# Kernel optimization log

Hardware: AMD Instinct MI355X
Metric: run time of the kernel (lower is better)

The kernel has to match this reference:

```python
import jax, jax.numpy as jnp
import numpy as np

B, N = 16, 2048
NOTE, BEAT_H, MEAS_H, FINAL_H = 512, 128, 64, 128
NUM_BEATS, NUM_MEAS = 256, 64
OUT = 11            # output_size; QPM_INDEX = 0
QPM = 0


def _uniform(k, shape, fan):
    b = 1.0 / np.sqrt(fan)
    return jax.random.uniform(k, shape, jnp.float32, -b, b)


def _lstm_cell(x, h, c, wih, whh, bih, bhh):
    g = x @ wih.T + bih + h @ whh.T + bhh
    ii, ff, gg, oo = jnp.split(g, 4, axis=-1)
    c2 = jax.nn.sigmoid(ff) * c + jax.nn.sigmoid(ii) * jnp.tanh(gg)
    return jax.nn.sigmoid(oo) * jnp.tanh(c2), c2


def setup_inputs() -> dict:
    key = jax.random.key(0)
    ks = jax.random.split(key, 20)
    note_emb = jax.random.normal(ks[0], (B, N, NOTE), jnp.float32)
    beat_emb = jax.random.normal(ks[1], (B, NUM_BEATS, BEAT_H), jnp.float32)
    measure_emb = jax.random.normal(ks[2], (B, NUM_MEAS, MEAS_H), jnp.float32)
    beat_numbers = jnp.sort(jax.random.randint(ks[3], (B, N), 0, NUM_BEATS), axis=1)
    measure_numbers = beat_numbers // (NUM_BEATS // NUM_MEAS)
    tin = BEAT_H + MEAS_H + 1 + (OUT - 1)   # beat-tempo LSTM input size
    fin = NOTE + BEAT_H + MEAS_H + OUT      # final LSTM input size
    d = OUT - 1
    return {
        "note_emb": note_emb, "beat_emb": beat_emb, "measure_emb": measure_emb,
        "beat_numbers": beat_numbers, "measure_numbers": measure_numbers,
        "Wa": _uniform(ks[4], (d, d), d), "ba": _uniform(ks[5], (d,), d),
        "ctx": _uniform(ks[6], (d,), d),
        "Wih_t": _uniform(ks[7], (4 * BEAT_H, tin), BEAT_H),
        "Whh_t": _uniform(ks[8], (4 * BEAT_H, BEAT_H), BEAT_H),
        "bih_t": _uniform(ks[9], (4 * BEAT_H,), BEAT_H),
        "bhh_t": _uniform(ks[10], (4 * BEAT_H,), BEAT_H),
        "Wih_f": _uniform(ks[11], (4 * FINAL_H, fin), FINAL_H),
        "Whh_f": _uniform(ks[12], (4 * FINAL_H, FINAL_H), FINAL_H),
        "bih_f": _uniform(ks[13], (4 * FINAL_H,), FINAL_H),
        "bhh_f": _uniform(ks[14], (4 * FINAL_H,), FINAL_H),
        "W_fc": _uniform(ks[15], (d, FINAL_H), FINAL_H),
        "b_fc": _uniform(ks[16], (d,), FINAL_H),
        "W_tfc": _uniform(ks[17], (1, BEAT_H), BEAT_H),
        "b_tfc": _uniform(ks[18], (1,), BEAT_H),
    }


def _decode(note_emb, beat_emb, measure_emb, beat_numbers, measure_numbers,
            Wa, ba, ctx, Wih_t, Whh_t, bih_t, bhh_t,
            Wih_f, Whh_f, bih_f, bhh_f, W_fc, b_fc, W_tfc, b_tfc):
    Bn, Nn = note_emb.shape[0], note_emb.shape[1]
    d = W_fc.shape[0]  # OUT - 1
    zs_beat = jnp.maximum(beat_numbers - beat_numbers[:, :1], 0)
    zs_meas = jnp.maximum(measure_numbers - measure_numbers[:, :1], 0)
    diff = jnp.diff(beat_numbers, axis=1)
    # beat_changed: first step forced to 1, then diff of beat numbers
    changed_all = jnp.concatenate([jnp.ones((Bn, 1), diff.dtype), diff], axis=1) > 0
    pos = jnp.arange(Nn)
    bidx = jnp.arange(Bn)

    carry0 = (
        jnp.zeros((Bn, BEAT_H)), jnp.zeros((Bn, BEAT_H)),        # tempo h, c
        jnp.zeros((Bn, FINAL_H)), jnp.zeros((Bn, FINAL_H)),      # final h, c
        jnp.zeros((Bn, d + 1)),                                   # prev_out
        jnp.zeros((Bn, beat_emb.shape[1], d)),                    # beat_results
        jnp.zeros((Bn, Nn, d + 1)),                               # out_total
    )

    def step(carry, i):
        th, tc, fh, fc_, prev_out, beat_results, out_total = carry
        changed = changed_all[:, i]                                # [B] bool
        # --- get_beat_corresp_out: notes j < i in the beat just finished ---
        prev_beat = beat_numbers[:, jnp.maximum(i - 1, 0)]         # [B]
        note_mask = (beat_numbers == prev_beat[:, None]) & (pos[None, :] < i)
        x = out_total[:, :, QPM + 1:]                              # [B,N,d]
        sim = (x @ Wa.T + ba) @ ctx                                # [B,N]
        sim = jnp.where(note_mask, sim, -1e9)
        w = jax.nn.softmax(sim, axis=1)
        result_node = jnp.einsum('bn,bnd->bd', w, x)
        result_node = jnp.where(note_mask.any(axis=1)[:, None], result_node, 0.0)
        cb = zs_beat[:, i]
        cm = zs_meas[:, i]
        # scatter result_node into beat_results only for batches whose beat changed
        old = beat_results[bidx, cb]
        beat_results = beat_results.at[bidx, cb].set(
            jnp.where(changed[:, None], result_node, old))
        # --- beat tempo RNN step (only applied where changed) ---
        tempo_in = jnp.concatenate([
            beat_emb[bidx, cb], measure_emb[bidx, cm],
            prev_out[:, QPM:QPM + 1], beat_results[bidx, cb]], axis=-1)
        th2, tc2 = _lstm_cell(tempo_in, th, tc, Wih_t, Whh_t, bih_t, bhh_t)
        th = jnp.where(changed[:, None], th2, th)
        tc = jnp.where(changed[:, None], tc2, tc)
        tmp_tempo = th2 @ W_tfc.T + b_tfc                          # [B,1]
        prev_out = prev_out.at[:, QPM:QPM + 1].set(
            jnp.where(changed[:, None], tmp_tempo, prev_out[:, QPM:QPM + 1]))
        # --- final note-level LSTM step (all batches) ---
        fin_in = jnp.concatenate([
            note_emb[:, i], beat_emb[bidx, cb], measure_emb[bidx, cm], prev_out], axis=-1)
        fh, fc_ = _lstm_cell(fin_in, fh, fc_, Wih_f, Whh_f, bih_f, bhh_f)
        out = fh @ W_fc.T + b_fc                                   # [B,d]
        prev_out = jnp.concatenate([prev_out[:, :QPM + 1], out], axis=-1)
        out_total = out_total.at[:, i].set(prev_out)
        return (th, tc, fh, fc_, prev_out, beat_results, out_total), None

    carry, _ = jax.lax.scan(step, carry0, jnp.arange(Nn))
    out_total = carry[-1]
    # zero out padded notes (note embedding all-zero rows)
    pad = (note_emb.sum(-1) == 0)[:, :, None]
    return jnp.where(pad, 0.0, out_total)


def reference(note_emb, beat_emb, measure_emb, beat_numbers, measure_numbers,
              Wa, ba, ctx, Wih_t, Whh_t, bih_t, bhh_t,
              Wih_f, Whh_f, bih_f, bhh_f, W_fc, b_fc, W_tfc, b_tfc):
    return _decode(note_emb, beat_emb, measure_emb, beat_numbers, measure_numbers,
                   Wa, ba, ctx, Wih_t, Whh_t, bih_t, bhh_t,
                   Wih_f, Whh_f, bih_f, bhh_f, W_fc, b_fc, W_tfc, b_tfc)
```

## Files before the change

kernel.cpp:

```cpp
#include <hip/hip_runtime.h>
#include <cstdint>
#include <cstddef>

#define B_      16
#define N_      2048
#define NOTE_   512
#define BEAT_H_ 128
#define MEAS_H_ 64
#define NBEATS_ 256
#define NMEAS_  64
#define OUT_    11
#define D_      10

typedef float f32x4 __attribute__((ext_vector_type(4)));
typedef unsigned int u32x4 __attribute__((ext_vector_type(4)));
typedef _Float16 h2v __attribute__((ext_vector_type(2)));

__device__ __forceinline__ float fexp2_(float x) {
#if __has_builtin(__builtin_amdgcn_exp2f)
    return __builtin_amdgcn_exp2f(x);
#else
    return exp2f(x);
#endif
}
__device__ __forceinline__ float frcp_(float x) {
#if __has_builtin(__builtin_amdgcn_rcpf)
    return __builtin_amdgcn_rcpf(x);
#else
    return 1.0f / x;
#endif
}
__device__ __forceinline__ float sigm_(float x) {
    return frcp_(1.0f + fexp2_(-1.4426950408889634f * x));
}
__device__ __forceinline__ float tanh_(float x) {
    return 1.0f - 2.0f * frcp_(fexp2_(2.8853900817779268f * x) + 1.0f);
}

__device__ __forceinline__ float dot2f_(unsigned wu, unsigned hu, float c) {
    union { unsigned u; h2v h; } a, bb;
    a.u = wu; bb.u = hu;
#if __has_builtin(__builtin_amdgcn_fdot2)
    return __builtin_amdgcn_fdot2(a.h, bb.h, c, false);
#else
    return c + (float)a.h[0] * (float)bb.h[0] + (float)a.h[1] * (float)bb.h[1];
#endif
}

#define BAR_LDS() asm volatile("s_waitcnt lgkmcnt(0)\n\ts_barrier" ::: "memory")

__device__ __forceinline__ void gstore16(void* p, _Float16 v) {
    *(__attribute__((address_space(1))) _Float16*)p = v;
}

__device__ __align__(16) _Float16 g_w_i16[512 * 128];
__device__ float g_bias_eff[512];
__device__ float g_wtail0[512];
__device__ __align__(16) _Float16 g_wht_i16[512 * 128];

__global__ __launch_bounds__(256) void pad_k(const float* __restrict__ note,
                                             int* __restrict__ padf) {
    int wave = threadIdx.x >> 6, lane = threadIdx.x & 63;
    int r = blockIdx.x * 4 + wave;
    const float* row = note + ((size_t)r << 9);
    float s = 0.f;
#pragma unroll
    for (int u = 0; u < 8; ++u) s += row[lane + (u << 6)];
#pragma unroll
    for (int off = 32; off; off >>= 1) s += __shfl_xor(s, off, 64);
    if (lane == 0) padf[r] = (s == 0.0f) ? 1 : 0;
}

__global__ __launch_bounds__(128) void fold_whh(
    const float* __restrict__ Whh_f, const float* __restrict__ Wih_f,
    const float* __restrict__ W_fc, const float* __restrict__ b_fc) {
    int gr = blockIdx.x;
    int t = threadIdx.x;
    __shared__ float tail[OUT_];
    if (t < OUT_) tail[t] = Wih_f[(size_t)gr * 715 + 704 + t];
    __syncthreads();
    float m = Whh_f[(size_t)gr * 128 + t];
#pragma unroll
    for (int d = 0; d < D_; ++d) m += tail[1 + d] * W_fc[d * 128 + t];
    int g = gr >> 7, e = gr & 127;
    int half = g >> 1, slot = g & 1;
    int gl = ((e >> 5) << 6) + (e & 31) + (half << 5);
    int k = slot * 16 + (t >> 3);
    g_w_i16[(size_t)(k * 256 + gl) * 8 + (t & 7)] = (_Float16)m;
    if (t == 0) {
        float bb = 0.f;
#pragma unroll
        for (int d = 0; d < D_; ++d) bb += tail[1 + d] * b_fc[d];
        g_bias_eff[gr] = bb;
        g_wtail0[gr] = tail[0];
    }
}

__global__ __launch_bounds__(128) void fold_wht(const float* __restrict__ Whh_t) {
    int gr = blockIdx.x, t = threadIdx.x;
    int g = gr >> 7, e = gr & 127;
    int half = g >> 1, slot = g & 1;
    int gl = ((e >> 5) << 6) + (e & 31) + (half << 5);
    int k = slot * 16 + (t >> 3);
    g_wht_i16[(size_t)(k * 256 + gl) * 8 + (t & 7)] = (_Float16)Whh_t[(size_t)gr * 128 + t];
}

__global__ __launch_bounds__(256) void tempo_pre_k(
    const float* __restrict__ beat, const float* __restrict__ meas,
    const int* __restrict__ bnum, const int* __restrict__ mnum,
    const float* __restrict__ Wih_t, const float* __restrict__ bih_t,
    const float* __restrict__ bhh_t, float* __restrict__ tpre) {
    __shared__ float sin_[16][192];
    int b = blockIdx.x, qt = blockIdx.y;
    int t = threadIdx.x;
    int bn0 = bnum[b << 11], mn0 = mnum[b << 11];
    for (int idx = t; idx < 16 * 192; idx += 256) {
        int qq = idx / 192, kk = idx - qq * 192;
        int q = qt * 16 + qq;
        float v;
        if (kk < 128) {
            v = beat[(size_t)(b * NBEATS_ + q) * 128 + kk];
        } else {
            int cm = ((q + bn0) >> 2) - mn0;
            if (cm > 63) cm = 63;
            if (cm < 0) cm = 0;
            v = meas[(size_t)(b * NMEAS_ + cm) * 64 + (kk - 128)];
        }
        sin_[qq][kk] = v;
    }
    __syncthreads();
    for (int half = 0; half < 2; ++half) {
        int c = t + half * 256;
        int j = ((c & 3) << 7) | (c >> 2);
        const float* wr = Wih_t + (size_t)j * 203;
        float bias = bih_t[j] + bhh_t[j];
        float acc[16] = {};
        for (int k = 0; k < 192; ++k) {
            float w = wr[k];
#pragma unroll
            for (int qq = 0; qq < 16; ++qq) acc[qq] += w * sin_[qq][k];
        }
        for (int qq = 0; qq < 16; ++qq)
            tpre[(size_t)(b * NBEATS_ + qt * 16 + qq) * 512 + c] = acc[qq] + bias;
    }
}

__global__ __launch_bounds__(256) void fin_pre_gemm(
    const float* __restrict__ note, const float* __restrict__ beat,
    const float* __restrict__ meas, const int* __restrict__ bnum,
    const int* __restrict__ mnum, const float* __restrict__ Wih_f,
    const float* __restrict__ bih_f, const float* __restrict__ bhh_f,
    float* __restrict__ finp) {
    __shared__ float As[16][64];
    __shared__ float Bs[16][64];
    int t = threadIdx.x;
    int r0 = blockIdx.x * 64;
    int j0 = blockIdx.y * 64;

    int am = t >> 2, alane = t & 3;
    int r = r0 + am;
    int b = r >> 11;
    int rb = b << 11;
    int cb = bnum[r] - bnum[rb];
    int cm = mnum[r] - mnum[rb];
    const float* arow_note = note + ((size_t)r << 9);
    const float* arow_beat = beat + ((size_t)(b * NBEATS_ + cb) << 7);
    const float* arow_meas = meas + ((size_t)(b * NMEAS_ + cm) << 6);

    int jj = t >> 2, blane = t & 3;
    int cB = j0 + jj;
    int jB = ((cB & 3) << 7) | (cB >> 2);
    const float* brow = Wih_f + (size_t)jB * 715;

    int tm0 = (t & 15) * 4, tn0 = (t >> 4) * 4;
    float acc[4][4] = {};

    for (int k0 = 0; k0 < 704; k0 += 16) {
        int ka = k0 + alane * 4;
        float4 av;
        if (ka < 512)      av = *(const float4*)(arow_note + ka);
        else if (ka < 640) av = *(const float4*)(arow_beat + (ka - 512));
        else               av = *(const float4*)(arow_meas + (ka - 640));
        int kb = k0 + blane * 4;
        float b0 = brow[kb], b1 = brow[kb + 1], b2 = brow[kb + 2], b3 = brow[kb + 3];
        __syncthreads();
        As[alane * 4 + 0][am] = av.x;
        As[alane * 4 + 1][am] = av.y;
        As[alane * 4 + 2][am] = av.z;
        As[alane * 4 + 3][am] = av.w;
        Bs[blane * 4 + 0][jj] = b0;
        Bs[blane * 4 + 1][jj] = b1;
        Bs[blane * 4 + 2][jj] = b2;
        Bs[blane * 4 + 3][jj] = b3;
        __syncthreads();
#pragma unroll
        for (int kk = 0; kk < 16; ++kk) {
            float4 a4 = *(const float4*)&As[kk][tm0];
            float4 b4 = *(const float4*)&Bs[kk][tn0];
            float aa[4] = {a4.x, a4.y, a4.z, a4.w};
            float bb[4] = {b4.x, b4.y, b4.z, b4.w};
#pragma unroll
            for (int mi = 0; mi < 4; ++mi)
#pragma unroll
                for (int ni = 0; ni < 4; ++ni) acc[mi][ni] += aa[mi] * bb[ni];
        }
    }
    float bias[4], beff[4];
#pragma unroll
    for (int ni = 0; ni < 4; ++ni) {
        int c = j0 + tn0 + ni;
        int j = ((c & 3) << 7) | (c >> 2);
        bias[ni] = bih_f[j] + bhh_f[j];
        beff[ni] = g_bias_eff[j];
    }
#pragma unroll
    for (int mi = 0; mi < 4; ++mi) {
        int rr = r0 + tm0 + mi;
        float eb = (rr & 2047) ? 1.0f : 0.0f;
        float4 o;
        o.x = acc[mi][0] + bias[0] + eb * beff[0];
        o.y = acc[mi][1] + bias[1] + eb * beff[1];
        o.z = acc[mi][2] + bias[2] + eb * beff[2];
        o.w = acc[mi][3] + bias[3] + eb * beff[3];
        *(float4*)(finp + ((size_t)rr << 9) + j0 + tn0) = o;
    }
}

__global__ __launch_bounds__(256)
__attribute__((amdgpu_waves_per_eu(1, 1)))
void decode_seq(
    float* finp,
    const float* __restrict__ tpre, const int* __restrict__ bnum,
    const float* __restrict__ Wih_t,
    const float* __restrict__ W_fc, const float* __restrict__ b_fc,
    const float* __restrict__ W_tfc, const float* __restrict__ b_tfc,
    const float* __restrict__ Wa, const float* __restrict__ ba,
    const float* __restrict__ ctx, float* __restrict__ tval) {
    __shared__ __align__(16) u32x4 wht_i_s[32 * 256];
    __shared__ __align__(16) _Float16 hbc16[2][128];
    __shared__ __align__(16) _Float16 ht16_s[128];
    __shared__ __align__(16) _Float16 u16_s[128];
    __shared__ __align__(16) float hA_s[128];
    __shared__ __align__(16) float s_w_s[1024];
    __shared__ float wfcT[128][12];
    __shared__ float bfc_s[12];
    __shared__ float v_s[12];
    __shared__ float cur_res[12];
    __shared__ float pred_s[4];
    __shared__ float sc_s[4];
    __shared__ unsigned short run_start_s[300];
    __shared__ short run_cb_s[300];
    __shared__ int nruns_s;

    const int t = threadIdx.x, l = t & 63, wid = t >> 6;
    const int b = blockIdx.x;
    const int half = l >> 5;
    const int e = wid * 32 + (l & 31);
    const int rowA = (half * 2) * 128 + e;
    const int rowB = (half * 2 + 1) * 128 + e;
    const float kmul = half ? 2.0f : 1.0f;
    const float badd = half ? -1.0f : 0.0f;

    const float* finb = finp + ((size_t)b << 11) * 512;
    char* hg = (char*)finb;
    const int colByte = (e << 4) + (half << 3);

    {
        const u32x4* src = (const u32x4*)g_wht_i16;
#pragma unroll
        for (int k2 = 0; k2 < 32; ++k2) wht_i_s[k2 * 256 + t] = src[k2 * 256 + t];
    }

    u32x4 wreg[32];
    {
        const u32x4* gw = (const u32x4*)g_w_i16;
#pragma unroll
        for (int k = 0; k < 32; ++k) wreg[k] = gw[k * 256 + t];
    }
    asm volatile("" : "+v"(wreg[0]), "+v"(wreg[1]), "+v"(wreg[2]), "+v"(wreg[3]),
                      "+v"(wreg[4]), "+v"(wreg[5]), "+v"(wreg[6]), "+v"(wreg[7]));
    asm volatile("" : "+v"(wreg[8]), "+v"(wreg[9]), "+v"(wreg[10]), "+v"(wreg[11]),
                      "+v"(wreg[12]), "+v"(wreg[13]), "+v"(wreg[14]), "+v"(wreg[15]));
    asm volatile("" : "+v"(wreg[16]), "+v"(wreg[17]), "+v"(wreg[18]), "+v"(wreg[19]),
                      "+v"(wreg[20]), "+v"(wreg[21]), "+v"(wreg[22]), "+v"(wreg[23]));
    asm volatile("" : "+v"(wreg[24]), "+v"(wreg[25]), "+v"(wreg[26]), "+v"(wreg[27]),
                      "+v"(wreg[28]), "+v"(wreg[29]), "+v"(wreg[30]), "+v"(wreg[31]));

    const float wt0A = g_wtail0[rowA];
    const float wt0B = g_wtail0[rowB];
    const float wtfc_r = W_tfc[e];
    const float btfc_r = b_tfc[0];
    float wiht0A = Wih_t[(size_t)rowA * 203 + 192];
    float wiht0B = Wih_t[(size_t)rowB * 203 + 192];
    float wihtdA[D_], wihtdB[D_];
#pragma unroll
    for (int d = 0; d < D_; ++d) {
        wihtdA[d] = Wih_t[(size_t)rowA * 203 + 193 + d];
        wihtdB[d] = Wih_t[(size_t)rowB * 203 + 193 + d];
    }

    for (int k = t; k < 128 * D_; k += 256) {
        int d = k >> 7, r = k & 127;
        wfcT[r][d] = W_fc[k];
    }
    if (t < 128) {
        hbc16[0][t] = (_Float16)0.f;
        hbc16[1][t] = (_Float16)0.f;
        ht16_s[t] = (_Float16)0.f;
    }
    if (t < D_) {
        bfc_s[t] = b_fc[t];
        cur_res[t] = 0.f;
        float vv = 0.f;
        for (int m = 0; m < D_; ++m) vv += ctx[m] * Wa[m * D_ + t];
        v_s[t] = vv;
    }
    if (t == 10) {
        float cc = 0.f;
        for (int m = 0; m < D_; ++m) cc += ba[m] * ctx[m];
        sc_s[0] = cc;
    }
    const int* bnb = bnum + (b << 11);
    int bn0 = bnb[0];
    int base = t * 8;
    int bv[8];
#pragma unroll
    for (int j = 0; j < 8; ++j) bv[j] = bnb[base + j];
    int prevv = base ? bnb[base - 1] : (bv[0] - 1);
    int c = 0;
    {
        int vv = prevv;
#pragma unroll
        for (int j = 0; j < 8; ++j) { c += (bv[j] != vv); vv = bv[j]; }
    }
    ((int*)s_w_s)[t] = c;
    __syncthreads();
    if (t == 0) {
        float c1v = sc_s[0];
        for (int d = 0; d < D_; ++d) c1v += bfc_s[d] * v_s[d];
        sc_s[3] = c1v;
    }
    if (t < 128) {
        float uu = 0.f;
#pragma unroll
        for (int d = 0; d < D_; ++d) uu += v_s[d] * wfcT[t][d];
        u16_s[t] = (_Float16)uu;
    }
    {
        int incl = c;
#pragma unroll
        for (int off = 1; off < 64; off <<= 1) {
            int n = __shfl_up(incl, off, 64);
            if (l >= off) incl += n;
        }
        if (l == 63) ((int*)s_w_s)[512 + wid] = incl;
        __syncthreads();
        int woff = 0;
        for (int w = 0; w < wid; ++w) woff += ((int*)s_w_s)[512 + w];
        int O = woff + incl - c;
        int vv = prevv;
#pragma unroll
        for (int j = 0; j < 8; ++j) {
            if (bv[j] != vv) {
                run_start_s[O] = (unsigned short)(base + j);
                run_cb_s[O] = (short)(bv[j] - bn0);
                O++;
            }
            vv = bv[j];
        }
        if (t == 0)
            nruns_s = ((int*)s_w_s)[512] + ((int*)s_w_s)[513] +
                      ((int*)s_w_s)[514] + ((int*)s_w_s)[515];
    }
    __syncthreads();
    const int nruns_r = nruns_s;

    float2 gf_cur = *(const float2*)((const char*)finb + colByte);
    float2 tp_cur = *(const float2*)((const char*)(tpre + (size_t)(b * NBEATS_) * 512) + colByte);
    int cur_run = -1, next_start = 0, run_s = 0, S_prev = 0;
    int pb = 0;
    float cf_r = 0.f, ct_r = 0.f;
    float prev0_r = 0.f;

#pragma unroll 1
    for (int i = 0; i < N_; ++i) {
        const bool changed = (i == next_start);
        if (changed) {
            ++cur_run;
            S_prev = run_s;
            run_s = i;
            next_start = (cur_run + 1 < nruns_r) ? (int)run_start_s[cur_run + 1] : (N_ * 2);
        }
        int inx = (i + 1 < N_) ? (i + 1) : i;
        float2 gf_nxt = *(const float2*)((const char*)finb + (size_t)inx * 2048 + colByte);

        float a0 = 0.f, a1 = 0.f, a2 = 0.f, a3 = 0.f;
        float b0 = 0.f, b1 = 0.f, b2 = 0.f, b3 = 0.f;
        {
            const u32x4* hq = (const u32x4*)&hbc16[pb][0];
#pragma unroll
            for (int k = 0; k < 16; ++k) {
                u32x4 H = hq[k];
                a0 = dot2f_(wreg[k].x, H.x, a0);
                a1 = dot2f_(wreg[k].y, H.y, a1);
                a2 = dot2f_(wreg[k].z, H.z, a2);
                a3 = dot2f_(wreg[k].w, H.w, a3);
                b0 = dot2f_(wreg[16 + k].x, H.x, b0);
                b1 = dot2f_(wreg[16 + k].y, H.y, b1);
                b2 = dot2f_(wreg[16 + k].z, H.z, b2);
                b3 = dot2f_(wreg[16 + k].w, H.w, b3);
            }
        }
        const float baseA = gf_cur.x + ((a0 + a1) + (a2 + a3));
        const float baseB = gf_cur.y + ((b0 + b1) + (b2 + b3));
        gf_cur = gf_nxt;
        float gA, gB, tv;

        if (!changed) {
            gA = baseA + wt0A * prev0_r;
            gB = baseB + wt0B * prev0_r;
            tv = prev0_r;
        } else {
            float t0 = 0.f, t1 = 0.f, t2 = 0.f, t3 = 0.f;
            float u0 = 0.f, u1 = 0.f, u2 = 0.f, u3 = 0.f;
            {
                const u32x4* htq = (const u32x4*)ht16_s;
#pragma unroll
                for (int k = 0; k < 16; ++k) {
                    u32x4 HT = htq[k];
                    u32x4 WA = wht_i_s[k * 256 + t];
                    u32x4 WB = wht_i_s[(16 + k) * 256 + t];
                    t0 = dot2f_(WA.x, HT.x, t0);
                    t1 = dot2f_(WA.y, HT.y, t1);
                    t2 = dot2f_(WA.z, HT.z, t2);
                    t3 = dot2f_(WA.w, HT.w, t3);
                    u0 = dot2f_(WB.x, HT.x, u0);
                    u1 = dot2f_(WB.y, HT.y, u1);
                    u2 = dot2f_(WB.z, HT.z, u2);
                    u3 = dot2f_(WB.w, HT.w, u3);
                }
            }
            float gtA = tp_cur.x + ((t0 + t1) + (t2 + t3)) + wiht0A * prev0_r;
            float gtB = tp_cur.y + ((u0 + u1) + (u2 + u3)) + wiht0B * prev0_r;
            if (cur_run + 1 < nruns_r) {
                int cb2 = (int)run_cb_s[cur_run + 1];
                tp_cur = *(const float2*)((const char*)(tpre + (size_t)(b * NBEATS_ + cb2) * 512) + colByte);
            }

            if (wid == 0) {
                int Lc = i - S_prev;
                if (Lc > 1024) Lc = 1024;
                const char* hgB = hg + (size_t)S_prev * 2048;
                const float c1 = sc_s[3];
                float lmax = -1e30f;
                for (int j = l; j < Lc; j += 64) {
                    const u32x4* hrow = (const u32x4*)(hgB + (size_t)j * 2048);
                    const u32x4* uq = (const u32x4*)u16_s;
                    float s0 = 0.f, s1 = 0.f, s2 = 0.f, s3 = 0.f;
#pragma unroll
                    for (int k = 0; k < 16; ++k) {
                        u32x4 hv = hrow[k], uv = uq[k];
                        s0 = dot2f_(hv.x, uv.x, s0);
                        s1 = dot2f_(hv.y, uv.y, s1);
                        s2 = dot2f_(hv.z, uv.z, s2);
                        s3 = dot2f_(hv.w, uv.w, s3);
                    }
                    float s = c1 + ((s0 + s1) + (s2 + s3));
                    s_w_s[j] = s;
                    lmax = fmaxf(lmax, s);
                }
#pragma unroll
                for (int off = 32; off; off >>= 1)
                    lmax = fmaxf(lmax, __shfl_xor(lmax, off, 64));
                float lsum = 0.f;
                for (int j = l; j < Lc; j += 64) {
                    float w = fexp2_(1.4426950408889634f * (s_w_s[j] - lmax));
                    s_w_s[j] = w;
                    lsum += w;
                }
#pragma unroll
                for (int off = 32; off; off >>= 1) lsum += __shfl_xor(lsum, off, 64);
                float inv = (Lc > 0) ? (1.0f / lsum) : 0.f;
                float hA0 = 0.f, hA1 = 0.f;
                for (int j = 0; j < Lc; ++j) {
                    unsigned hv = *(const unsigned*)(hgB + (size_t)j * 2048 + (l << 2));
                    float w = s_w_s[j];
                    union { unsigned u; _Float16 h[2]; } hu; hu.u = hv;
                    hA0 += w * (float)hu.h[0];
                    hA1 += w * (float)hu.h[1];
                }
                hA_s[2 * l] = hA0 * inv;
                hA_s[2 * l + 1] = hA1 * inv;
                int dd = l >> 3, rl = l & 7, d2 = 8 + dd;
                float po1 = 0.f, po2 = 0.f;
                for (int k2 = 0; k2 < 16; ++k2) {
                    int r = rl + (k2 << 3);
                    float hv = hA_s[r];
                    po1 += hv * wfcT[r][dd];
                    if (d2 < D_) po2 += hv * wfcT[r][d2];
                }
                po1 += __shfl_xor(po1, 1, 64); po1 += __shfl_xor(po1, 2, 64); po1 += __shfl_xor(po1, 4, 64);
                po2 += __shfl_xor(po2, 1, 64); po2 += __shfl_xor(po2, 2, 64); po2 += __shfl_xor(po2, 4, 64);
                if (rl == 0) {
                    cur_res[dd] = (Lc > 0) ? (po1 + bfc_s[dd]) : 0.f;
                    if (d2 < D_) cur_res[d2] = (Lc > 0) ? (po2 + bfc_s[d2]) : 0.f;
                }
            }
            BAR_LDS();
#pragma unroll
            for (int d = 0; d < D_; ++d) {
                float cr = cur_res[d];
                gtA += wihtdA[d] * cr;
                gtB += wihtdB[d] * cr;
            }
            float actA = fmaf(kmul, sigm_(kmul * gtA), badd);
            float actB = sigm_(gtB);
            float shA = __shfl_xor(actA, 32, 64);
            float shB = __shfl_xor(actB, 32, 64);
            float p = 0.f;
            if (l < 32) {
                float c2 = actB * ct_r + actA * shA;
                float h2 = shB * tanh_(c2);
                ct_r = c2;
                ht16_s[e] = (_Float16)h2;
                p = h2 * wtfc_r;
            }
            p += __shfl_xor(p, 1, 64);
            p += __shfl_xor(p, 2, 64);
            p += __shfl_xor(p, 4, 64);
            p += __shfl_xor(p, 8, 64);
            p += __shfl_xor(p, 16, 64);
            if (l == 0) pred_s[wid] = p;
            BAR_LDS();
            float tnew = btfc_r + pred_s[0] + pred_s[1] + pred_s[2] + pred_s[3];
            prev0_r = tnew;
            tv = tnew;
            gA = baseA + wt0A * tnew;
            gB = baseB + wt0B * tnew;
        }

        {
            float actA = fmaf(kmul, sigm_(kmul * gA), badd);
            float actB = sigm_(gB);
            float shA = __shfl_xor(actA, 32, 64);
            float shB = __shfl_xor(actB, 32, 64);
            if (l < 32) {
                float c2 = actB * cf_r + actA * shA;
                float h2 = shB * tanh_(c2);
                cf_r = c2;
                hbc16[pb ^ 1][e] = (_Float16)h2;
                gstore16(hg + ((size_t)i << 11) + (e << 1), (_Float16)h2);
            }
        }
        if (t == 0) tval[(b << 11) + i] = tv;
        if (i + 1 == next_start) __syncthreads();
        else BAR_LDS();
        pb ^= 1;
    }
}

__global__ __launch_bounds__(256) void out_k(
    const float* __restrict__ finp, const float* __restrict__ tval,
    const int* __restrict__ padf, const float* __restrict__ W_fc,
    const float* __restrict__ b_fc, float* __restrict__ out) {
    int g = blockIdx.x * 256 + threadIdx.x;
    int row = g >> 4, slot = g & 15;
    if (row >= B_ * N_) return;
    int pd = padf[row];
    float* orow = out + (size_t)row * OUT_;
    if (slot == 10) {
        orow[0] = pd ? 0.f : tval[row];
        return;
    }
    if (slot > 10) return;
    const unsigned* h2 = (const unsigned*)(finp + (size_t)row * 512);
    const float* wr = W_fc + slot * 128;
    float acc = b_fc[slot];
#pragma unroll 8
    for (int k = 0; k < 64; ++k) {
        union { unsigned u; _Float16 h[2]; } hv; hv.u = h2[k];
        acc += (float)hv.h[0] * wr[2 * k] + (float)hv.h[1] * wr[2 * k + 1];
    }
    orow[1 + slot] = pd ? 0.f : acc;
}

extern "C" void kernel_launch(void* const* d_in, const int* in_sizes, int n_in,
                              void* d_out, int out_size, void* d_ws, size_t ws_size,
                              hipStream_t stream) {
    const float* note  = (const float*)d_in[0];
    const float* beat  = (const float*)d_in[1];
    const float* meas  = (const float*)d_in[2];
    const int*   bnum  = (const int*)d_in[3];
    const int*   mnum  = (const int*)d_in[4];
    const float* Wa    = (const float*)d_in[5];
    const float* ba    = (const float*)d_in[6];
    const float* ctx   = (const float*)d_in[7];
    const float* Wih_t = (const float*)d_in[8];
    const float* Whh_t = (const float*)d_in[9];
    const float* bih_t = (const float*)d_in[10];
    const float* bhh_t = (const float*)d_in[11];
    const float* Wih_f = (const float*)d_in[12];
    const float* Whh_f = (const float*)d_in[13];
    const float* bih_f = (const float*)d_in[14];
    const float* bhh_f = (const float*)d_in[15];
    const float* W_fc  = (const float*)d_in[16];
    const float* b_fc  = (const float*)d_in[17];
    const float* W_tfc = (const float*)d_in[18];
    const float* b_tfc = (const float*)d_in[19];
    float* out = (float*)d_out;

    char* ws = (char*)d_ws;
    float* finp = (float*)ws;
    float* tpre = (float*)(ws + (size_t)64 * 1024 * 1024);
    int*   padf = (int*)(ws + (size_t)72 * 1024 * 1024);
    float* tval = (float*)(ws + (size_t)73 * 1024 * 1024);

    pad_k<<<8192, 256, 0, stream>>>(note, padf);
    fold_whh<<<512, 128, 0, stream>>>(Whh_f, Wih_f, W_fc, b_fc);
    fold_wht<<<512, 128, 0, stream>>>(Whh_t);
    tempo_pre_k<<<dim3(16, 16), 256, 0, stream>>>(beat, meas, bnum, mnum, Wih_t,
                                                  bih_t, bhh_t, tpre);
    fin_pre_gemm<<<dim3(512, 8), 256, 0, stream>>>(note, beat, meas, bnum, mnum,
                                                   Wih_f, bih_f, bhh_f, finp);
    decode_seq<<<16, 256, 0, stream>>>(finp, tpre, bnum, Wih_t,
                                       W_fc, b_fc, W_tfc, b_tfc, Wa, ba, ctx,
                                       tval);
    out_k<<<2048, 256, 0, stream>>>(finp, tval, padf, W_fc, b_fc, out);
}
```

Before: 3.895 ms.

## Keep recent note hidden states in an LDS ring buffer for beat attention

Replaces the double-buffered hidden state with a 64-row LDS ring of recent final-LSTM hidden states. Beat-level attention over short runs (up to 64 notes) then reads from LDS in a single-pass, per-lane softmax instead of reading the global scratch with multiple passes. Long runs fall back to the old global path behind a full __syncthreads. Also moves W_fc columns into registers, issues the LDS loads ahead of the dot products, and drops the conditional full barrier at run ends. In exchange it uses more LDS and registers, which could cause spilling.

After: 3.877 ms. No clear change (-0.5%).

```diff
diff --git a/kernel.cpp b/kernel.cpp
--- a/kernel.cpp
+++ b/kernel.cpp
@@ -11,6 +11,8 @@
 #define NMEAS_  64
 #define OUT_    11
 #define D_      10
+#define RING_   64
+#define RSTR_   136
 
 typedef float f32x4 __attribute__((ext_vector_type(4)));
 typedef unsigned int u32x4 __attribute__((ext_vector_type(4)));
@@ -52,6 +54,17 @@
 __device__ __forceinline__ void gstore16(void* p, _Float16 v) {
     *(__attribute__((address_space(1))) _Float16*)p = v;
 }
+
+#define F8(a,b,c,d,e,f,g,h) \
+    asm volatile("" : "+v"(a),"+v"(b),"+v"(c),"+v"(d),"+v"(e),"+v"(f),"+v"(g),"+v"(h))
+
+#define LD16(V, P, S)                                                         \
+    u32x4 V##0=(P)[0*(S)],  V##1=(P)[1*(S)],  V##2=(P)[2*(S)],  V##3=(P)[3*(S)],  \
+          V##4=(P)[4*(S)],  V##5=(P)[5*(S)],  V##6=(P)[6*(S)],  V##7=(P)[7*(S)],  \
+          V##8=(P)[8*(S)],  V##9=(P)[9*(S)],  V##10=(P)[10*(S)], V##11=(P)[11*(S)],\
+          V##12=(P)[12*(S)], V##13=(P)[13*(S)], V##14=(P)[14*(S)], V##15=(P)[15*(S)];\
+    F8(V##0,V##1,V##2,V##3,V##4,V##5,V##6,V##7);                              \
+    F8(V##8,V##9,V##10,V##11,V##12,V##13,V##14,V##15);
 
 __device__ __align__(16) _Float16 g_w_i16[512 * 128];
 __device__ float g_bias_eff[512];
@@ -237,12 +250,11 @@
     const float* __restrict__ Wa, const float* __restrict__ ba,
     const float* __restrict__ ctx, float* __restrict__ tval) {
     __shared__ __align__(16) u32x4 wht_i_s[32 * 256];
-    __shared__ __align__(16) _Float16 hbc16[2][128];
+    __shared__ __align__(16) _Float16 ring_s[RING_][RSTR_];
     __shared__ __align__(16) _Float16 ht16_s[128];
     __shared__ __align__(16) _Float16 u16_s[128];
     __shared__ __align__(16) float hA_s[128];
     __shared__ __align__(16) float s_w_s[1024];
-    __shared__ float wfcT[128][12];
     __shared__ float bfc_s[12];
     __shared__ float v_s[12];
     __shared__ float cur_res[12];
@@ -263,7 +275,7 @@
 
     const float* finb = finp + ((size_t)b << 11) * 512;
     char* hg = (char*)finb;
-    const int colByte = (e << 4) + (half << 3);
+    const int colf = (e << 2) + (half << 1);
 
     {
         const u32x4* src = (const u32x4*)g_wht_i16;
@@ -277,14 +289,10 @@
 #pragma unroll
         for (int k = 0; k < 32; ++k) wreg[k] = gw[k * 256 + t];
     }
-    asm volatile("" : "+v"(wreg[0]), "+v"(wreg[1]), "+v"(wreg[2]), "+v"(wreg[3]),
-                      "+v"(wreg[4]), "+v"(wreg[5]), "+v"(wreg[6]), "+v"(wreg[7]));
-    asm volatile("" : "+v"(wreg[8]), "+v"(wreg[9]), "+v"(wreg[10]), "+v"(wreg[11]),
-                      "+v"(wreg[12]), "+v"(wreg[13]), "+v"(wreg[14]), "+v"(wreg[15]));
-    asm volatile("" : "+v"(wreg[16]), "+v"(wreg[17]), "+v"(wreg[18]), "+v"(wreg[19]),
-                      "+v"(wreg[20]), "+v"(wreg[21]), "+v"(wreg[22]), "+v"(wreg[23]));
-    asm volatile("" : "+v"(wreg[24]), "+v"(wreg[25]), "+v"(wreg[26]), "+v"(wreg[27]),
-                      "+v"(wreg[28]), "+v"(wreg[29]), "+v"(wreg[30]), "+v"(wreg[31]));
+    F8(wreg[0], wreg[1], wreg[2], wreg[3], wreg[4], wreg[5], wreg[6], wreg[7]);
+    F8(wreg[8], wreg[9], wreg[10], wreg[11], wreg[12], wreg[13], wreg[14], wreg[15]);
+    F8(wreg[16], wreg[17], wreg[18], wreg[19], wreg[20], wreg[21], wreg[22], wreg[23]);
+    F8(wreg[24], wreg[25], wreg[26], wreg[27], wreg[28], wreg[29], wreg[30], wreg[31]);
 
     const float wt0A = g_wtail0[rowA];
     const float wt0B = g_wtail0[rowB];
@@ -298,16 +306,16 @@
         wihtdA[d] = Wih_t[(size_t)rowA * 203 + 193 + d];
         wihtdB[d] = Wih_t[(size_t)rowB * 203 + 193 + d];
     }
-
-    for (int k = t; k < 128 * D_; k += 256) {
-        int d = k >> 7, r = k & 127;
-        wfcT[r][d] = W_fc[k];
-    }
-    if (t < 128) {
-        hbc16[0][t] = (_Float16)0.f;
-        hbc16[1][t] = (_Float16)0.f;
-        ht16_s[t] = (_Float16)0.f;
-    }
+    const int dd_ = l >> 3, rl_ = l & 7, d2_ = dd_ + 8;
+    float wfcA[16], wfcB[16];
+#pragma unroll
+    for (int k2 = 0; k2 < 16; ++k2) {
+        wfcA[k2] = W_fc[dd_ * 128 + rl_ + 8 * k2];
+        wfcB[k2] = (d2_ < D_) ? W_fc[d2_ * 128 + rl_ + 8 * k2] : 0.f;
+    }
+
+    if (t < 128) ht16_s[t] = (_Float16)0.f;
+    if (t < 64) *(unsigned*)&ring_s[RING_ - 1][2 * t] = 0u;
     if (t < D_) {
         bfc_s[t] = b_fc[t];
         cur_res[t] = 0.f;
@@ -343,7 +351,7 @@
     if (t < 128) {
         float uu = 0.f;
 #pragma unroll
-        for (int d = 0; d < D_; ++d) uu += v_s[d] * wfcT[t][d];
+        for (int d = 0; d < D_; ++d) uu += v_s[d] * W_fc[d * 128 + t];
         u16_s[t] = (_Float16)uu;
     }
     {
@@ -375,10 +383,9 @@
     __syncthreads();
     const int nruns_r = nruns_s;
 
-    float2 gf_cur = *(const float2*)((const char*)finb + colByte);
-    float2 tp_cur = *(const float2*)((const char*)(tpre + (size_t)(b * NBEATS_) * 512) + colByte);
+    float2 gf_cur = *(const float2*)(finb + colf);
+    float2 tp_cur = *(const float2*)(tpre + (size_t)(b * NBEATS_) * 512 + colf);
     int cur_run = -1, next_start = 0, run_s = 0, S_prev = 0;
-    int pb = 0;
     float cf_r = 0.f, ct_r = 0.f;
     float prev0_r = 0.f;
 
@@ -391,29 +398,35 @@
             run_s = i;
             next_start = (cur_run + 1 < nruns_r) ? (int)run_start_s[cur_run + 1] : (N_ * 2);
         }
-        int inx = (i + 1 < N_) ? (i + 1) : i;
-        float2 gf_nxt = *(const float2*)((const char*)finb + (size_t)inx * 2048 + colByte);
-
-        float a0 = 0.f, a1 = 0.f, a2 = 0.f, a3 = 0.f;
-        float b0 = 0.f, b1 = 0.f, b2 = 0.f, b3 = 0.f;
+        const float gx = gf_cur.x, gy = gf_cur.y;
         {
-            const u32x4* hq = (const u32x4*)&hbc16[pb][0];
-#pragma unroll
-            for (int k = 0; k < 16; ++k) {
-                u32x4 H = hq[k];
-                a0 = dot2f_(wreg[k].x, H.x, a0);
-                a1 = dot2f_(wreg[k].y, H.y, a1);
-                a2 = dot2f_(wreg[k].z, H.z, a2);
-                a3 = dot2f_(wreg[k].w, H.w, a3);
-                b0 = dot2f_(wreg[16 + k].x, H.x, b0);
-                b1 = dot2f_(wreg[16 + k].y, H.y, b1);
-                b2 = dot2f_(wreg[16 + k].z, H.z, b2);
-                b3 = dot2f_(wreg[16 + k].w, H.w, b3);
-            }
-        }
-        const float baseA = gf_cur.x + ((a0 + a1) + (a2 + a3));
-        const float baseB = gf_cur.y + ((b0 + b1) + (b2 + b3));
-        gf_cur = gf_nxt;
+            int inx = (i + 1 < N_) ? (i + 1) : i;
+            gf_cur = *(const float2*)(finb + (size_t)inx * 512 + colf);
+        }
+
+        float accA, accB;
+        {
+            const u32x4* hq = (const u32x4*)&ring_s[(i + RING_ - 1) & (RING_ - 1)][0];
+            LD16(H, hq, 1)
+            float a0 = 0.f, a1 = 0.f, a2 = 0.f, a3 = 0.f;
+            float b0 = 0.f, b1 = 0.f, b2 = 0.f, b3 = 0.f;
+#define MM(K)                                                   \
+            a0 = dot2f_(wreg[K].x, H##K.x, a0);                 \
+            a1 = dot2f_(wreg[K].y, H##K.y, a1);                 \
+            a2 = dot2f_(wreg[K].z, H##K.z, a2);                 \
+            a3 = dot2f_(wreg[K].w, H##K.w, a3);                 \
+            b0 = dot2f_(wreg[16 + K].x, H##K.x, b0);            \
+            b1 = dot2f_(wreg[16 + K].y, H##K.y, b1);            \
+            b2 = dot2f_(wreg[16 + K].z, H##K.z, b2);            \
+            b3 = dot2f_(wreg[16 + K].w, H##K.w, b3);
+            MM(0) MM(1) MM(2) MM(3) MM(4) MM(5) MM(6) MM(7)
+            MM(8) MM(9) MM(10) MM(11) MM(12) MM(13) MM(14) MM(15)
+#undef MM
+            accA = (a0 + a1) + (a2 + a3);
+            accB = (b0 + b1) + (b2 + b3);
+        }
+        const float baseA = gx + accA;
+        const float baseB = gy + accB;
         float gA, gB, tv;
 
         if (!changed) {
@@ -421,89 +434,165 @@
             gB = baseB + wt0B * prev0_r;
             tv = prev0_r;
         } else {
-            float t0 = 0.f, t1 = 0.f, t2 = 0.f, t3 = 0.f;
-            float u0 = 0.f, u1 = 0.f, u2 = 0.f, u3 = 0.f;
+            const int Lc = i - S_prev;
+            const bool longrun = Lc > RING_;
+            if (longrun) __syncthreads();
+            const float tx = tp_cur.x, ty = tp_cur.y;
+
+            float gtA, gtB;
             {
                 const u32x4* htq = (const u32x4*)ht16_s;
-#pragma unroll
-                for (int k = 0; k < 16; ++k) {
-                    u32x4 HT = htq[k];
-                    u32x4 WA = wht_i_s[k * 256 + t];
-                    u32x4 WB = wht_i_s[(16 + k) * 256 + t];
-                    t0 = dot2f_(WA.x, HT.x, t0);
-                    t1 = dot2f_(WA.y, HT.y, t1);
-                    t2 = dot2f_(WA.z, HT.z, t2);
-                    t3 = dot2f_(WA.w, HT.w, t3);
-                    u0 = dot2f_(WB.x, HT.x, u0);
-                    u1 = dot2f_(WB.y, HT.y, u1);
-                    u2 = dot2f_(WB.z, HT.z, u2);
-                    u3 = dot2f_(WB.w, HT.w, u3);
+                LD16(HT, htq, 1)
+                const u32x4* wta = (const u32x4*)wht_i_s + t;
+                float q0 = 0.f, q1 = 0.f, q2 = 0.f, q3 = 0.f;
+                {
+                    LD16(WA, wta, 256)
+#define TT(K, W)                                                \
+                    q0 = dot2f_(W##K.x, HT##K.x, q0);           \
+                    q1 = dot2f_(W##K.y, HT##K.y, q1);           \
+                    q2 = dot2f_(W##K.z, HT##K.z, q2);           \
+                    q3 = dot2f_(W##K.w, HT##K.w, q3);
+                    TT(0, WA) TT(1, WA) TT(2, WA) TT(3, WA)
+                    TT(4, WA) TT(5, WA) TT(6, WA) TT(7, WA)
+                    TT(8, WA) TT(9, WA) TT(10, WA) TT(11, WA)
+                    TT(12, WA) TT(13, WA) TT(14, WA) TT(15, WA)
                 }
+                gtA = tx + ((q0 + q1) + (q2 + q3)) + wiht0A * prev0_r;
+                q0 = q1 = q2 = q3 = 0.f;
+                {
+                    LD16(WB, (wta + 16 * 256), 256)
+                    TT(0, WB) TT(1, WB) TT(2, WB) TT(3, WB)
+                    TT(4, WB) TT(5, WB) TT(6, WB) TT(7, WB)
+                    TT(8, WB) TT(9, WB) TT(10, WB) TT(11, WB)
+                    TT(12, WB) TT(13, WB) TT(14, WB) TT(15, WB)
+#undef TT
+                }
+                gtB = ty + ((q0 + q1) + (q2 + q3)) + wiht0B * prev0_r;
             }
-            float gtA = tp_cur.x + ((t0 + t1) + (t2 + t3)) + wiht0A * prev0_r;
-            float gtB = tp_cur.y + ((u0 + u1) + (u2 + u3)) + wiht0B * prev0_r;
             if (cur_run + 1 < nruns_r) {
                 int cb2 = (int)run_cb_s[cur_run + 1];
-                tp_cur = *(const float2*)((const char*)(tpre + (size_t)(b * NBEATS_ + cb2) * 512) + colByte);
+                tp_cur = *(const float2*)(tpre + (size_t)(b * NBEATS_ + cb2) * 512 + colf);
             }
 
             if (wid == 0) {
-                int Lc = i - S_prev;
-                if (Lc > 1024) Lc = 1024;
-                const char* hgB = hg + (size_t)S_prev * 2048;
                 const float c1 = sc_s[3];
-                float lmax = -1e30f;
-                for (int j = l; j < Lc; j += 64) {
-                    const u32x4* hrow = (const u32x4*)(hgB + (size_t)j * 2048);
-                    const u32x4* uq = (const u32x4*)u16_s;
-                    float s0 = 0.f, s1 = 0.f, s2 = 0.f, s3 = 0.f;
-#pragma unroll
-                    for (int k = 0; k < 16; ++k) {
-                        u32x4 hv = hrow[k], uv = uq[k];
-                        s0 = dot2f_(hv.x, uv.x, s0);
-                        s1 = dot2f_(hv.y, uv.y, s1);
-                        s2 = dot2f_(hv.z, uv.z, s2);
-                        s3 = dot2f_(hv.w, uv.w, s3);
+                if (!longrun) {
+                    float sc;
+                    {
+                        const u32x4* uqp = (const u32x4*)u16_s;
+                        LD16(UU, uqp, 1)
+                        int sj = (S_prev + l) & (RING_ - 1);
+                        const u32x4* hr = (const u32x4*)&ring_s[sj][0];
+                        LD16(RH, hr, 1)
+                        float s0 = 0.f, s1 = 0.f, s2 = 0.f, s3 = 0.f;
+#define SCD(K)                                                  \
+                        s0 = dot2f_(RH##K.x, UU##K.x, s0);      \
+                        s1 = dot2f_(RH##K.y, UU##K.y, s1);      \
+                        s2 = dot2f_(RH##K.z, UU##K.z, s2);      \
+                        s3 = dot2f_(RH##K.w, UU##K.w, s3);
+                        SCD(0) SCD(1) SCD(2) SCD(3) SCD(4) SCD(5) SCD(6) SCD(7)
+                        SCD(8) SCD(9) SCD(10) SCD(11) SCD(12) SCD(13) SCD(14) SCD(15)
+#undef SCD
+                        sc = (l < Lc) ? (c1 + ((s0 + s1) + (s2 + s3))) : -1e30f;
                     }
-                    float s = c1 + ((s0 + s1) + (s2 + s3));
-                    s_w_s[j] = s;
-                    lmax = fmaxf(lmax, s);
+                    float mx = sc;
+#pragma unroll
+                    for (int off = 32; off; off >>= 1)
+                        mx = fmaxf(mx, __shfl_xor(mx, off, 64));
+                    float w = (l < Lc) ? fexp2_(1.4426950408889634f * (sc - mx)) : 0.f;
+                    float sm = w;
+#pragma unroll
+                    for (int off = 32; off; off >>= 1) sm += __shfl_xor(sm, off, 64);
+                    s_w_s[l] = w;
+                    float inv = (Lc > 0) ? frcp_(sm) : 0.f;
+                    float hA0 = 0.f, hA1 = 0.f;
+                    int jj = 0;
+                    for (; jj + 4 <= Lc; jj += 4) {
+                        unsigned x0 = *(const unsigned*)&ring_s[(S_prev + jj) & (RING_ - 1)][2 * l];
+                        unsigned x1 = *(const unsigned*)&ring_s[(S_prev + jj + 1) & (RING_ - 1)][2 * l];
+                        unsigned x2 = *(const unsigned*)&ring_s[(S_prev + jj + 2) & (RING_ - 1)][2 * l];
+                        unsigned x3 = *(const unsigned*)&ring_s[(S_prev + jj + 3) & (RING_ - 1)][2 * l];
+                        float w0 = s_w_s[jj], w1 = s_w_s[jj + 1];
+                        float w2 = s_w_s[jj + 2], w3 = s_w_s[jj + 3];
+                        union { unsigned u; _Float16 h[2]; } y0, y1, y2, y3;
+                        y0.u = x0; y1.u = x1; y2.u = x2; y3.u = x3;
+                        hA0 += w0 * (float)y0.h[0] + w1 * (float)y1.h[0] +
+                               w2 * (float)y2.h[0] + w3 * (float)y3.h[0];
+                        hA1 += w0 * (float)y0.h[1] + w1 * (float)y1.h[1] +
+                               w2 * (float)y2.h[1] + w3 * (float)y3.h[1];
+                    }
+                    for (; jj < Lc; ++jj) {
+                        unsigned x0 = *(const unsigned*)&ring_s[(S_prev + jj) & (RING_ - 1)][2 * l];
+                        float w0 = s_w_s[jj];
+                        union { unsigned u; _Float16 h[2]; } y0; y0.u = x0;
+                        hA0 += w0 * (float)y0.h[0];
+                        hA1 += w0 * (float)y0.h[1];
+                    }
+                    float2 hw; hw.x = hA0 * inv; hw.y = hA1 * inv;
+                    *(float2*)&hA_s[2 * l] = hw;
+                } else {
+                    int Lcc = Lc;
+                    if (Lcc > 1024) Lcc = 1024;
+                    const char* hgB = hg + (size_t)S_prev * 2048;
+                    const u32x4* uqp = (const u32x4*)u16_s;
+                    LD16(UU, uqp, 1)
+                    float lmax = -1e30f;
+                    for (int j = l; j < Lcc; j += 64) {
+                        const u32x4* hrow = (const u32x4*)(hgB + (size_t)j * 2048);
+                        LD16(RH, hrow, 1)
+                        float s0 = 0.f, s1 = 0.f, s2 = 0.f, s3 = 0.f;
+#define SCD(K)                                                  \
+                        s0 = dot2f_(RH##K.x, UU##K.x, s0);      \
+                        s1 = dot2f_(RH##K.y, UU##K.y, s1);      \
+                        s2 = dot2f_(RH##K.z, UU##K.z, s2);      \
+                        s3 = dot2f_(RH##K.w, UU##K.w, s3);
+                        SCD(0) SCD(1) SCD(2) SCD(3) SCD(4) SCD(5) SCD(6) SCD(7)
+                        SCD(8) SCD(9) SCD(10) SCD(11) SCD(12) SCD(13) SCD(14) SCD(15)
+#undef SCD
+                        float s = c1 + ((s0 + s1) + (s2 + s3));
+                        s_w_s[j] = s;
+                        lmax = fmaxf(lmax, s);
+                    }
+#pragma unroll
+                    for (int off = 32; off; off >>= 1)
+                        lmax = fmaxf(lmax, __shfl_xor(lmax, off, 64));
+                    float lsum = 0.f;
+                    for (int j = l; j < Lcc; j += 64) {
+                        float w = fexp2_(1.4426950408889634f * (s_w_s[j] - lmax));
+                        s_w_s[j] = w;
+                        lsum += w;
+                    }
+#pragma unroll
+                    for (int off = 32; off; off >>= 1) lsum += __shfl_xor(lsum, off, 64);
+                    float inv = frcp_(lsum);
+                    float hA0 = 0.f, hA1 = 0.f;
+                    for (int j = 0; j < Lcc; ++j) {
+                        unsigned hv = *(const unsigned*)(hgB + (size_t)j * 2048 + (l << 2));
+                        float w = s_w_s[j];
+                        union { unsigned u; _Float16 h[2]; } hu; hu.u = hv;
+                        hA0 += w * (float)hu.h[0];
+                        hA1 += w * (float)hu.h[1];
+                    }
+                    float2 hw; hw.x = hA0 * inv; hw.y = hA1 * inv;
+                    *(float2*)&hA_s[2 * l] = hw;
                 }
-#pragma unroll
-                for (int off = 32; off; off >>= 1)
-                    lmax = fmaxf(lmax, __shfl_xor(lmax, off, 64));
-                float lsum = 0.f;
-                for (int j = l; j < Lc; j += 64) {
-                    float w = fexp2_(1.4426950408889634f * (s_w_s[j] - lmax));
-                    s_w_s[j] = w;
-                    lsum += w;
-                }
-#pragma unroll
-                for (int off = 32; off; off >>= 1) lsum += __shfl_xor(lsum, off, 64);
-                float inv = (Lc > 0) ? (1.0f / lsum) : 0.f;
-                float hA0 = 0.f, hA1 = 0.f;
-                for (int j = 0; j < Lc; ++j) {
-                    unsigned hv = *(const unsigned*)(hgB + (size_t)j * 2048 + (l << 2));
-                    float w = s_w_s[j];
-                    union { unsigned u; _Float16 h[2]; } hu; hu.u = hv;
-                    hA0 += w * (float)hu.h[0];
-                    hA1 += w * (float)hu.h[1];
-                }
-                hA_s[2 * l] = hA0 * inv;
-                hA_s[2 * l + 1] = hA1 * inv;
-                int dd = l >> 3, rl = l & 7, d2 = 8 + dd;
                 float po1 = 0.f, po2 = 0.f;
-                for (int k2 = 0; k2 < 16; ++k2) {
-                    int r = rl + (k2 << 3);
-                    float hv = hA_s[r];
-                    po1 += hv * wfcT[r][dd];
-                    if (d2 < D_) po2 += hv * wfcT[r][d2];
+#pragma unroll
+                for (int g4 = 0; g4 < 4; ++g4) {
+                    float h0 = hA_s[rl_ + g4 * 32 + 0];
+                    float h1 = hA_s[rl_ + g4 * 32 + 8];
+                    float h2 = hA_s[rl_ + g4 * 32 + 16];
+                    float h3 = hA_s[rl_ + g4 * 32 + 24];
+                    po1 += h0 * wfcA[4 * g4] + h1 * wfcA[4 * g4 + 1] +
+                           h2 * wfcA[4 * g4 + 2] + h3 * wfcA[4 * g4 + 3];
+                    po2 += h0 * wfcB[4 * g4] + h1 * wfcB[4 * g4 + 1] +
+                           h2 * wfcB[4 * g4 + 2] + h3 * wfcB[4 * g4 + 3];
                 }
                 po1 += __shfl_xor(po1, 1, 64); po1 += __shfl_xor(po1, 2, 64); po1 += __shfl_xor(po1, 4, 64);
                 po2 += __shfl_xor(po2, 1, 64); po2 += __shfl_xor(po2, 2, 64); po2 += __shfl_xor(po2, 4, 64);
-                if (rl == 0) {
-                    cur_res[dd] = (Lc > 0) ? (po1 + bfc_s[dd]) : 0.f;
-                    if (d2 < D_) cur_res[d2] = (Lc > 0) ? (po2 + bfc_s[d2]) : 0.f;
+                if (rl_ == 0) {
+                    cur_res[dd_] = (Lc > 0) ? (po1 + bfc_s[dd_]) : 0.f;
+                    if (d2_ < D_) cur_res[d2_] = (Lc > 0) ? (po2 + bfc_s[d2_]) : 0.f;
                 }
             }
             BAR_LDS();
@@ -548,14 +637,12 @@
                 float c2 = actB * cf_r + actA * shA;
                 float h2 = shB * tanh_(c2);
                 cf_r = c2;
-                hbc16[pb ^ 1][e] = (_Float16)h2;
+                ring_s[i & (RING_ - 1)][e] = (_Float16)h2;
                 gstore16(hg + ((size_t)i << 11) + (e << 1), (_Float16)h2);
             }
         }
         if (t == 0) tval[(b << 11) + i] = tv;
-        if (i + 1 == next_start) __syncthreads();
-        else BAR_LDS();
-        pb ^= 1;
+        BAR_LDS();
     }
 }
 
```
